# Optimization experiments

Hardware: AMD Instinct MI355X
Metric: run time of the kernel (lower is better)

Reference implementation:

```python
import jax, jax.numpy as jnp
import numpy as np

N_NODES = 100000
N_EDGES = 1600000
F_IN = 64
N_HID = 64
N_CLS = 40
K = 2  # kernel_size, degree-1 open B-spline in 1-D pseudo-coordinate


def setup_inputs() -> dict:
    key = jax.random.key(0)
    ks = jax.random.split(key, 8)
    x = jax.random.normal(ks[0], (N_NODES, F_IN), dtype=jnp.float32)
    edge_index = jax.random.randint(ks[1], (2, N_EDGES), 0, N_NODES, dtype=jnp.int32)
    edge_attr = jax.random.uniform(ks[2], (N_EDGES, 1), dtype=jnp.float32)
    s1 = 1.0 / np.sqrt(F_IN)
    s2 = 1.0 / np.sqrt(N_HID)
    W1 = jax.random.normal(ks[3], (K, F_IN, N_HID), dtype=jnp.float32) * s1
    root1 = jax.random.normal(ks[4], (F_IN, N_HID), dtype=jnp.float32) * s1
    b1 = jnp.zeros((N_HID,), dtype=jnp.float32)
    W2 = jax.random.normal(ks[5], (K, N_HID, N_CLS), dtype=jnp.float32) * s2
    root2 = jax.random.normal(ks[6], (N_HID, N_CLS), dtype=jnp.float32) * s2
    b2 = jnp.zeros((N_CLS,), dtype=jnp.float32)
    return {"x": x, "edge_index": edge_index, "edge_attr": edge_attr,
            "W1": W1, "root1": root1, "b1": b1,
            "W2": W2, "root2": root2, "b2": b2}


def spline_conv(x, src, dst, u, W, root, b):
    """SplineConv, dim=1, kernel_size=2, degree=1, open spline, aggr='mean'.

    Degree-1 open spline with K=2: frac = u*(K-1) = u, basis weights are
    (1-u) at kernel index 0 and u at kernel index 1 for u in [0,1).
    Transform nodes once per kernel index, then gather+mix per edge (cheaper
    and mathematically identical to per-edge matmuls since basis scalars
    commute with the linear map).
    """
    h = jnp.einsum('nf,kfo->kno', x, W)  # [K, N, out]
    b1f = u[:, 0]                        # fractional basis weight, [E]
    msg = (1.0 - b1f)[:, None] * h[0][src] + b1f[:, None] * h[1][src]  # [E, out]
    agg = jax.ops.segment_sum(msg, dst, num_segments=x.shape[0])
    deg = jax.ops.segment_sum(jnp.ones_like(b1f), dst, num_segments=x.shape[0])
    agg = agg / jnp.maximum(deg, 1.0)[:, None]  # mean aggregation
    return agg + x @ root + b


def reference(x, edge_index, edge_attr, W1, root1, b1, W2, root2, b2):
    src, dst = edge_index[0], edge_index[1]
    # eval mode: F.dropout(training=False) is identity
    h = jax.nn.elu(spline_conv(x, src, dst, edge_attr, W1, root1, b1))
    out = spline_conv(h, src, dst, edge_attr, W2, root2, b2)
    return jax.nn.log_softmax(out, axis=1)
```

## Files before the change

### kernel.cpp

```cpp
#include <hip/hip_runtime.h>
#include <math.h>

#define N_NODES 100000
#define N_EDGES 1600000
#define NB_SCAN 391
#define CHUNK 4096
#define NCHA 391
#define NBUK 256
#define DPB 391
#define BSTRIDE 7168
#define TILE_N 25000

typedef __attribute__((ext_vector_type(8))) short bf16x8;
typedef __attribute__((ext_vector_type(4))) float f32x4;

__device__ __forceinline__ unsigned short f2bf(float f) {
    union { float f; unsigned u; } v; v.f = f;
    unsigned r = v.u + 0x7FFF + ((v.u >> 16) & 1);
    return (unsigned short)(r >> 16);
}
__device__ __forceinline__ float bf2f(unsigned short b) {
    union { unsigned u; float f; } v; v.u = ((unsigned)b) << 16;
    return v.f;
}

__global__ void x2bf16_kernel(const float* __restrict__ x,
                              unsigned short* __restrict__ xb) {
    int i = blockIdx.x * 256 + threadIdx.x;
    if (i >= N_NODES * 16) return;
    float4 v = reinterpret_cast<const float4*>(x)[i];
    ushort4 o;
    o.x = f2bf(v.x); o.y = f2bf(v.y); o.z = f2bf(v.z); o.w = f2bf(v.w);
    reinterpret_cast<ushort4*>(xb)[i] = o;
}

__global__ void wt_kernel(const float* __restrict__ W, const float* __restrict__ root,
                          unsigned short* __restrict__ Wt, int COUT, int total) {
    int i = blockIdx.x * 256 + threadIdx.x;
    if (i >= total) return;
    int c = i / 192;
    int k = i - c * 192;
    float v = 0.0f;
    if (c < COUT)
        v = (k < 128) ? W[(k >> 6) * 64 * COUT + (k & 63) * COUT + c]
                      : root[(k - 128) * COUT + c];
    Wt[i] = f2bf(v);
}

__global__ __launch_bounds__(256) void bin_edges(const int* __restrict__ ei,
                                                 const float* __restrict__ ea,
                                                 int* __restrict__ bucket_cur,
                                                 int2* __restrict__ binned) {
    __shared__ int hist[NBUK];
    __shared__ int lbase[NBUK];
    __shared__ int lcur[NBUK];
    __shared__ int gbase[NBUK];
    __shared__ int2 stage[CHUNK];
    __shared__ unsigned char sbkt[CHUNK];
    int tid = threadIdx.x;
    int e0 = blockIdx.x * CHUNK;
    int nval = min(CHUNK, N_EDGES - e0);

    if (tid < NBUK) hist[tid] = 0;
    __syncthreads();
    for (int j = tid; j < nval; j += 256)
        atomicAdd(&hist[ei[N_EDGES + e0 + j] / DPB], 1);
    __syncthreads();
    if (tid < NBUK) lbase[tid] = hist[tid];
    __syncthreads();
    for (int off = 1; off < NBUK; off <<= 1) {
        int v = (tid < NBUK && tid >= off) ? lbase[tid - off] : 0;
        __syncthreads();
        if (tid < NBUK) lbase[tid] += v;
        __syncthreads();
    }
    if (tid < NBUK) {
        int ex = lbase[tid] - hist[tid];
        lbase[tid] = ex;
        lcur[tid]  = ex;
        gbase[tid] = atomicAdd(&bucket_cur[tid], hist[tid]);
    }
    __syncthreads();
    for (int j = tid; j < nval; j += 256) {
        int e = e0 + j;
        int d = ei[N_EDGES + e];
        int b = d / DPB;
        int dl = d - b * DPB;
        float u = ea[e];
        int uq = min((int)(u * 65536.0f + 0.5f), 65535);
        int pos = atomicAdd(&lcur[b], 1);
        stage[pos] = make_int2(ei[e], (uq << 16) | dl);
        sbkt[pos] = (unsigned char)b;
    }
    __syncthreads();
    for (int j = tid; j < nval; j += 256) {
        int b = sbkt[j];
        int gp = gbase[b] + (j - lbase[b]);
        if (gp < BSTRIDE)
            binned[(size_t)b * BSTRIDE + gp] = stage[j];
    }
}

__global__ __launch_bounds__(512) void bucket_sort(const int* __restrict__ bucket_cur,
                                                   const int2* __restrict__ binned,
                                                   int2* __restrict__ rec,
                                                   int* __restrict__ rowptr,
                                                   int* __restrict__ cnt_g) {
    __shared__ int keycnt[1600];
    __shared__ int tsum[512];
    __shared__ int2 stage[BSTRIDE];
    int tid = threadIdx.x;
    int b = blockIdx.x;

    tsum[tid] = (tid < NBUK) ? bucket_cur[tid] : 0;
    __syncthreads();
    for (int off = 1; off < 512; off <<= 1) {
        int v = (tid >= off) ? tsum[tid - off] : 0;
        __syncthreads();
        tsum[tid] += v;
        __syncthreads();
    }
    int base = (b == 0) ? 0 : tsum[b - 1];
    int m = min(bucket_cur[b], BSTRIDE);
    __syncthreads();

    for (int k = tid; k < 1600; k += 512) keycnt[k] = 0;
    __syncthreads();
    const int2* bin = binned + (size_t)b * BSTRIDE;
    for (int j = tid; j < m; j += 512) {
        int2 r = bin[j];
        int key = ((r.y & 1023) << 2) | ((unsigned)r.x / TILE_N);
        atomicAdd(&keycnt[key], 1);
    }
    __syncthreads();
    int k0 = tid << 2;
    int c0 = 0, c1 = 0, c2 = 0, c3 = 0;
    if (tid < DPB) {
        c0 = keycnt[k0]; c1 = keycnt[k0 + 1];
        c2 = keycnt[k0 + 2]; c3 = keycnt[k0 + 3];
    }
    int s4 = c0 + c1 + c2 + c3;
    tsum[tid] = s4;
    __syncthreads();
    for (int off = 1; off < 512; off <<= 1) {
        int v = (tid >= off) ? tsum[tid - off] : 0;
        __syncthreads();
        tsum[tid] += v;
        __syncthreads();
    }
    if (tid < DPB) {
        int p = tsum[tid] - s4;
        int d = b * DPB + tid;
        if (d < N_NODES) {
            rowptr[d] = base + p;
            cnt_g[d]  = s4;
        }
        keycnt[k0] = p;     p += c0;
        keycnt[k0 + 1] = p; p += c1;
        keycnt[k0 + 2] = p; p += c2;
        keycnt[k0 + 3] = p;
    }
    __syncthreads();
    for (int j = tid; j < m; j += 512) {
        int2 r = bin[j];
        int key = ((r.y & 1023) << 2) | ((unsigned)r.x / TILE_N);
        float u = ((unsigned)r.y >> 16) * (1.0f / 65536.0f);
        int pos = atomicAdd(&keycnt[key], 1);
        if (pos < BSTRIDE) stage[pos] = make_int2(r.x, __float_as_int(u));
    }
    __syncthreads();
    for (int j = tid; j < m; j += 512)
        rec[base + j] = stage[j];
}

__global__ __launch_bounds__(256) void pull_agg(
        const int* __restrict__ rowptr, const int* __restrict__ cnt,
        const int2* __restrict__ rec, const unsigned short* __restrict__ featb,
        unsigned short* __restrict__ s01b) {
    int wave_id = (blockIdx.x * 256 + threadIdx.x) >> 6;
    int lane = threadIdx.x & 63;
    int fg = lane & 7;
    int eg = lane >> 3;
    int n = wave_id * 8 + eg;
    bool valid = n < N_NODES;
    int start = 0, deg = 0;
    if (valid) { start = rowptr[n]; deg = cnt[n]; }
    int end = start + deg;
    int il  = end - 1;
    const bf16x8* f8 = reinterpret_cast<const bf16x8*>(featb);
    float s[8], a1[8];
#pragma unroll
    for (int k = 0; k < 8; ++k) { s[k] = 0.0f; a1[k] = 0.0f; }

#define LD(IDX, R, V)                                              \
    { int ic = min(IDX, il); R = rec[ic];                          \
      V = f8[((size_t)(unsigned)R.x << 3) + fg]; }
#define MATH(IDX, R, V)                                            \
    { float mk = (IDX < end) ? 1.0f : 0.0f;                        \
      float um = mk * __int_as_float(R.y);                         \
      _Pragma("unroll")                                            \
      for (int t = 0; t < 8; ++t) {                                \
          float vv = bf2f((unsigned short)V[t]);                   \
          s[t]  = fmaf(mk, vv, s[t]);                              \
          a1[t] = fmaf(um, vv, a1[t]);                             \
      } }

    if (deg > 0) {
        int i = start;
        int2 r0, r1, r2, r3; bf16x8 v0, v1, v2, v3;
        LD(i,     r0, v0)
        LD(i + 1, r1, v1)
        LD(i + 2, r2, v2)
        LD(i + 3, r3, v3)
        while (true) {
            int j = i + 4;
            bool more = j < end;
            int2 q0, q1, q2, q3; bf16x8 w0, w1, w2, w3;
            if (more) {
                LD(j,     q0, w0)
                LD(j + 1, q1, w1)
                LD(j + 2, q2, w2)
                LD(j + 3, q3, w3)
            }
            MATH(i,     r0, v0)
            MATH(i + 1, r1, v1)
            MATH(i + 2, r2, v2)
            MATH(i + 3, r3, v3)
            if (!more) break;
            i = j;
            r0 = q0; v0 = w0; r1 = q1; v1 = w1;
            r2 = q2; v2 = w2; r3 = q3; v3 = w3;
        }
    }
#undef LD
#undef MATH

    if (valid) {
        float dinv = 1.0f / fmaxf((float)deg, 1.0f);
        bf16x8 o0, o1;
#pragma unroll
        for (int k = 0; k < 8; ++k) {
            o0[k] = (short)f2bf((s[k] - a1[k]) * dinv);
            o1[k] = (short)f2bf(a1[k] * dinv);
        }
        *reinterpret_cast<bf16x8*>(s01b + (size_t)n * 128 + fg * 8) = o0;
        *reinterpret_cast<bf16x8*>(s01b + (size_t)n * 128 + 64 + fg * 8) = o1;
    }
}

template<int COUT, int CT, int ACT>
__global__ __launch_bounds__(256) void gemm_mfma(
        const unsigned short* __restrict__ s01b,
        const unsigned short* __restrict__ featb,
        const unsigned short* __restrict__ Wt,
        const float* __restrict__ bias, void* __restrict__ outv) {
    int lane = threadIdx.x & 63;
    int wave = threadIdx.x >> 6;
    int l15  = lane & 15;
    int g    = lane >> 4;
    int nodebase = blockIdx.x * 256 + wave * 64;

    f32x4 acc[4][CT];
#pragma unroll
    for (int rt = 0; rt < 4; ++rt)
#pragma unroll
        for (int ct = 0; ct < CT; ++ct) acc[rt][ct] = (f32x4){0.f, 0.f, 0.f, 0.f};

#pragma unroll
    for (int ks = 0; ks < 6; ++ks) {
        int kk = ks * 32 + g * 8;
        bf16x8 zfrag[4];
#pragma unroll
        for (int rt = 0; rt < 4; ++rt) {
            int n = nodebase + rt * 16 + l15;
            if (n >= N_NODES) n = N_NODES - 1;
            const unsigned short* p = (kk < 128)
                ? (s01b + (size_t)n * 128 + kk)
                : (featb + (size_t)n * 64 + (kk - 128));
            zfrag[rt] = *reinterpret_cast<const bf16x8*>(p);
        }
        bf16x8 wfrag[CT];
#pragma unroll
        for (int ct = 0; ct < CT; ++ct)
            wfrag[ct] = *reinterpret_cast<const bf16x8*>(Wt + (size_t)(ct * 16 + l15) * 192 + kk);
#pragma unroll
        for (int rt = 0; rt < 4; ++rt)
#pragma unroll
            for (int ct = 0; ct < CT; ++ct)
                acc[rt][ct] = __builtin_amdgcn_mfma_f32_16x16x32_bf16(
                    wfrag[ct], zfrag[rt], acc[rt][ct], 0, 0, 0);
    }

    f32x4 bv[CT];
#pragma unroll
    for (int ct = 0; ct < CT; ++ct) {
        int base = ct * 16 + g * 4;
        if (base + 4 <= COUT) {
            float4 b = *reinterpret_cast<const float4*>(bias + base);
            bv[ct] = (f32x4){b.x, b.y, b.z, b.w};
        } else {
            bv[ct] = (f32x4){0.f, 0.f, 0.f, 0.f};
        }
    }

    if (ACT == 1) {
        unsigned short* out = (unsigned short*)outv;
#pragma unroll
        for (int rt = 0; rt < 4; ++rt) {
            int n = nodebase + rt * 16 + l15;
            if (n >= N_NODES) continue;
#pragma unroll
            for (int ct = 0; ct < CT; ++ct) {
                f32x4 v = acc[rt][ct] + bv[ct];
                ushort4 o;
                float e;
                e = v[0]; o.x = f2bf(e > 0.f ? e : expm1f(e));
                e = v[1]; o.y = f2bf(e > 0.f ? e : expm1f(e));
                e = v[2]; o.z = f2bf(e > 0.f ? e : expm1f(e));
                e = v[3]; o.w = f2bf(e > 0.f ? e : expm1f(e));
                *reinterpret_cast<ushort4*>(out + (size_t)n * 64 + ct * 16 + g * 4) = o;
            }
        }
    } else {
        float* out = (float*)outv;
#pragma unroll
        for (int rt = 0; rt < 4; ++rt) {
            int n = nodebase + rt * 16 + l15;
            float v[CT * 4];
            float m = -3.4e38f;
#pragma unroll
            for (int ct = 0; ct < CT; ++ct)
#pragma unroll
                for (int r = 0; r < 4; ++r) {
                    int ch = ct * 16 + g * 4 + r;
                    float t = acc[rt][ct][r] + bv[ct][r];
                    v[ct * 4 + r] = t;
                    if (ch < COUT) m = fmaxf(m, t);
                }
            m = fmaxf(m, __shfl_xor(m, 16));
            m = fmaxf(m, __shfl_xor(m, 32));
            float s = 0.0f;
#pragma unroll
            for (int ct = 0; ct < CT; ++ct)
#pragma unroll
                for (int r = 0; r < 4; ++r) {
                    int ch = ct * 16 + g * 4 + r;
                    if (ch < COUT) s += expf(v[ct * 4 + r] - m);
                }
            s += __shfl_xor(s, 16);
            s += __shfl_xor(s, 32);
            float lse = m + logf(s);
            if (n >= N_NODES) continue;
#pragma unroll
            for (int ct = 0; ct < CT; ++ct) {
                int base = ct * 16 + g * 4;
                if (base + 4 <= COUT) {
                    float4 o;
                    o.x = v[ct * 4 + 0] - lse;
                    o.y = v[ct * 4 + 1] - lse;
                    o.z = v[ct * 4 + 2] - lse;
                    o.w = v[ct * 4 + 3] - lse;
                    *reinterpret_cast<float4*>(out + (size_t)n * COUT + base) = o;
                }
            }
        }
    }
}

extern "C" void kernel_launch(void* const* d_in, const int* in_sizes, int n_in,
                              void* d_out, int out_size, void* d_ws, size_t ws_size,
                              hipStream_t stream) {
    const float* x     = (const float*)d_in[0];
    const int*   ei    = (const int*)d_in[1];
    const float* ea    = (const float*)d_in[2];
    const float* W1    = (const float*)d_in[3];
    const float* root1 = (const float*)d_in[4];
    const float* b1    = (const float*)d_in[5];
    const float* W2    = (const float*)d_in[6];
    const float* root2 = (const float*)d_in[7];
    const float* b2    = (const float*)d_in[8];
    float* out = (float*)d_out;

    char* p = (char*)d_ws;
    int*   bucket_cur = (int*)p;            p += 512 * 4;
    int2*  binned  = (int2*)p;              p += (size_t)NBUK * BSTRIDE * 8;
    int2*  rec     = (int2*)p;              p += (size_t)N_EDGES * 8;
    int*   rowptr  = (int*)p;               p += (size_t)N_NODES * 4;
    int*   cnt     = (int*)p;               p += (size_t)N_NODES * 4;
    unsigned short* s01b = (unsigned short*)p;  p += (size_t)N_NODES * 128 * 2;
    unsigned short* xb   = (unsigned short*)p;  p += (size_t)N_NODES * 64 * 2;
    unsigned short* hprb = (unsigned short*)p;  p += (size_t)N_NODES * 64 * 2;
    unsigned short* Wt1  = (unsigned short*)p;  p += (size_t)64 * 192 * 2;
    unsigned short* Wt2  = (unsigned short*)p;  p += (size_t)48 * 192 * 2;

    x2bf16_kernel<<<(N_NODES * 16) / 256, 256, 0, stream>>>(x, xb);
    wt_kernel<<<48, 256, 0, stream>>>(W1, root1, Wt1, 64, 64 * 192);
    wt_kernel<<<36, 256, 0, stream>>>(W2, root2, Wt2, 40, 48 * 192);
    hipMemsetAsync(bucket_cur, 0, 512 * 4, stream);

    bin_edges<<<NCHA, 256, 0, stream>>>(ei, ea, bucket_cur, binned);
    bucket_sort<<<NBUK, 512, 0, stream>>>(bucket_cur, binned, rec, rowptr, cnt);

    pull_agg<<<(N_NODES + 31) / 32, 256, 0, stream>>>(rowptr, cnt, rec, xb, s01b);
    gemm_mfma<64, 4, 1><<<NB_SCAN, 256, 0, stream>>>(s01b, xb, Wt1, b1, hprb);

    pull_agg<<<(N_NODES + 31) / 32, 256, 0, stream>>>(rowptr, cnt, rec, hprb, s01b);
    gemm_mfma<40, 3, 2><<<NB_SCAN, 256, 0, stream>>>(s01b, hprb, Wt2, b2, out);
}
```

Measured before the change: 163.4 us.

## Degree-bin node permutation for pull_agg and pack edge records to 32 bits

bucket_sort now builds a histogram of node degrees (capped at 63), and two new kernels, scan64 and perm_scatter, produce a permutation that groups nodes of similar degree. pull_agg walks nodes in that order, so the 8 nodes sharing a wave have similar loop trip counts and less divergence. Edge records are also packed into 32 bits (17-bit source plus 15-bit quantised u) instead of an int2, halving record traffic. The cost is two extra small launches, an indirection through perm, coarser quantisation of u, and loss of node locality when reading rowptr and cnt.

New measurement: 168.7 us. +3.3%, slower.

```diff
diff --git a/kernel.cpp b/kernel.cpp
--- a/kernel.cpp
+++ b/kernel.cpp
@@ -103,12 +103,16 @@
 
 __global__ __launch_bounds__(512) void bucket_sort(const int* __restrict__ bucket_cur,
                                                    const int2* __restrict__ binned,
-                                                   int2* __restrict__ rec,
+                                                   unsigned* __restrict__ rec,
                                                    int* __restrict__ rowptr,
-                                                   int* __restrict__ cnt_g) {
+                                                   int* __restrict__ cnt_g,
+                                                   int* __restrict__ bin_cnt,
+                                                   int* __restrict__ bin_rel,
+                                                   int* __restrict__ nodeinfo) {
     __shared__ int keycnt[1600];
     __shared__ int tsum[512];
-    __shared__ int2 stage[BSTRIDE];
+    __shared__ int dh[64];
+    __shared__ unsigned stage[BSTRIDE];
     int tid = threadIdx.x;
     int b = blockIdx.x;
 
@@ -125,6 +129,7 @@
     __syncthreads();
 
     for (int k = tid; k < 1600; k += 512) keycnt[k] = 0;
+    if (tid < 64) dh[tid] = 0;
     __syncthreads();
     const int2* bin = binned + (size_t)b * BSTRIDE;
     for (int j = tid; j < m; j += 512) {
@@ -148,6 +153,8 @@
         tsum[tid] += v;
         __syncthreads();
     }
+    bool isnode = (tid < DPB) && (b * DPB + tid < N_NODES);
+    int binid = 0, lpos = 0;
     if (tid < DPB) {
         int p = tsum[tid] - s4;
         int d = b * DPB + tid;
@@ -159,32 +166,67 @@
         keycnt[k0 + 1] = p; p += c1;
         keycnt[k0 + 2] = p; p += c2;
         keycnt[k0 + 3] = p;
-    }
-    __syncthreads();
+        if (isnode) {
+            binid = min(s4, 63);
+            lpos = atomicAdd(&dh[binid], 1);
+        }
+    }
+    __syncthreads();
+    if (tid < 64) bin_rel[b * 64 + tid] = atomicAdd(&bin_cnt[tid], dh[tid]);
+    if (isnode) nodeinfo[b * DPB + tid] = (binid << 9) | lpos;
     for (int j = tid; j < m; j += 512) {
         int2 r = bin[j];
         int key = ((r.y & 1023) << 2) | ((unsigned)r.x / TILE_N);
-        float u = ((unsigned)r.y >> 16) * (1.0f / 65536.0f);
+        unsigned uq15 = ((unsigned)r.y >> 17);
         int pos = atomicAdd(&keycnt[key], 1);
-        if (pos < BSTRIDE) stage[pos] = make_int2(r.x, __float_as_int(u));
+        if (pos < BSTRIDE) stage[pos] = ((unsigned)r.x << 15) | uq15;
     }
     __syncthreads();
     for (int j = tid; j < m; j += 512)
         rec[base + j] = stage[j];
 }
 
+__global__ void scan64(const int* __restrict__ bin_cnt, int* __restrict__ bin_base) {
+    __shared__ int s[64];
+    int t = threadIdx.x;
+    int v = bin_cnt[t];
+    s[t] = v;
+    __syncthreads();
+    for (int off = 1; off < 64; off <<= 1) {
+        int w = (t >= off) ? s[t - off] : 0;
+        __syncthreads();
+        s[t] += w;
+        __syncthreads();
+    }
+    bin_base[t] = s[t] - v;
+}
+
+__global__ void perm_scatter(const int* __restrict__ nodeinfo,
+                             const int* __restrict__ bin_rel,
+                             const int* __restrict__ bin_base,
+                             int* __restrict__ perm) {
+    int n = blockIdx.x * 256 + threadIdx.x;
+    if (n >= N_NODES) return;
+    int b = n / DPB;
+    int info = nodeinfo[n];
+    int bin = info >> 9;
+    int lpos = info & 511;
+    perm[bin_base[bin] + bin_rel[b * 64 + bin] + lpos] = n;
+}
+
 __global__ __launch_bounds__(256) void pull_agg(
         const int* __restrict__ rowptr, const int* __restrict__ cnt,
-        const int2* __restrict__ rec, const unsigned short* __restrict__ featb,
+        const int* __restrict__ perm, const unsigned* __restrict__ rec,
+        const unsigned short* __restrict__ featb,
         unsigned short* __restrict__ s01b) {
-    int wave_id = (blockIdx.x * 256 + threadIdx.x) >> 6;
+    int gid = (blockIdx.x * 256 + threadIdx.x) >> 6;
     int lane = threadIdx.x & 63;
     int fg = lane & 7;
     int eg = lane >> 3;
-    int n = wave_id * 8 + eg;
-    bool valid = n < N_NODES;
-    int start = 0, deg = 0;
-    if (valid) { start = rowptr[n]; deg = cnt[n]; }
+    int idx = gid * 8 + eg;
+    bool valid = idx < N_NODES;
+    int n = 0, start = 0, deg = 0;
+    if (valid) { n = perm[idx]; start = rowptr[n]; deg = cnt[n]; }
     int end = start + deg;
     int il  = end - 1;
     const bf16x8* f8 = reinterpret_cast<const bf16x8*>(featb);
@@ -194,10 +236,10 @@
 
 #define LD(IDX, R, V)                                              \
     { int ic = min(IDX, il); R = rec[ic];                          \
-      V = f8[((size_t)(unsigned)R.x << 3) + fg]; }
+      V = f8[((size_t)(R >> 15) << 3) + fg]; }
 #define MATH(IDX, R, V)                                            \
     { float mk = (IDX < end) ? 1.0f : 0.0f;                        \
-      float um = mk * __int_as_float(R.y);                         \
+      float um = mk * (float)(R & 0x7FFFu) * (1.0f / 32768.0f);    \
       _Pragma("unroll")                                            \
       for (int t = 0; t < 8; ++t) {                                \
           float vv = bf2f((unsigned short)V[t]);                   \
@@ -207,7 +249,7 @@
 
     if (deg > 0) {
         int i = start;
-        int2 r0, r1, r2, r3; bf16x8 v0, v1, v2, v3;
+        unsigned r0, r1, r2, r3; bf16x8 v0, v1, v2, v3;
         LD(i,     r0, v0)
         LD(i + 1, r1, v1)
         LD(i + 2, r2, v2)
@@ -215,7 +257,7 @@
         while (true) {
             int j = i + 4;
             bool more = j < end;
-            int2 q0, q1, q2, q3; bf16x8 w0, w1, w2, w3;
+            unsigned q0, q1, q2, q3; bf16x8 w0, w1, w2, w3;
             if (more) {
                 LD(j,     q0, w0)
                 LD(j + 1, q1, w1)
@@ -383,8 +425,13 @@
 
     char* p = (char*)d_ws;
     int*   bucket_cur = (int*)p;            p += 512 * 4;
+    int*   bin_cnt  = (int*)p;              p += 64 * 4;
+    int*   bin_base = (int*)p;              p += 64 * 4;
+    int*   bin_rel  = (int*)p;              p += (size_t)NBUK * 64 * 4;
+    int*   nodeinfo = (int*)p;              p += (size_t)N_NODES * 4;
+    int*   perm     = (int*)p;              p += (size_t)N_NODES * 4;
     int2*  binned  = (int2*)p;              p += (size_t)NBUK * BSTRIDE * 8;
-    int2*  rec     = (int2*)p;              p += (size_t)N_EDGES * 8;
+    unsigned* rec  = (unsigned*)p;          p += (size_t)N_EDGES * 4;
     int*   rowptr  = (int*)p;               p += (size_t)N_NODES * 4;
     int*   cnt     = (int*)p;               p += (size_t)N_NODES * 4;
     unsigned short* s01b = (unsigned short*)p;  p += (size_t)N_NODES * 128 * 2;
@@ -396,14 +443,17 @@
     x2bf16_kernel<<<(N_NODES * 16) / 256, 256, 0, stream>>>(x, xb);
     wt_kernel<<<48, 256, 0, stream>>>(W1, root1, Wt1, 64, 64 * 192);
     wt_kernel<<<36, 256, 0, stream>>>(W2, root2, Wt2, 40, 48 * 192);
-    hipMemsetAsync(bucket_cur, 0, 512 * 4, stream);
+    hipMemsetAsync(bucket_cur, 0, (512 + 64) * 4, stream);
 
     bin_edges<<<NCHA, 256, 0, stream>>>(ei, ea, bucket_cur, binned);
-    bucket_sort<<<NBUK, 512, 0, stream>>>(bucket_cur, binned, rec, rowptr, cnt);
-
-    pull_agg<<<(N_NODES + 31) / 32, 256, 0, stream>>>(rowptr, cnt, rec, xb, s01b);
+    bucket_sort<<<NBUK, 512, 0, stream>>>(bucket_cur, binned, rec, rowptr, cnt,
+                                          bin_cnt, bin_rel, nodeinfo);
+    scan64<<<1, 64, 0, stream>>>(bin_cnt, bin_base);
+    perm_scatter<<<NB_SCAN, 256, 0, stream>>>(nodeinfo, bin_rel, bin_base, perm);
+
+    pull_agg<<<(N_NODES + 31) / 32, 256, 0, stream>>>(rowptr, cnt, perm, rec, xb, s01b);
     gemm_mfma<64, 4, 1><<<NB_SCAN, 256, 0, stream>>>(s01b, xb, Wt1, b1, hprb);
 
-    pull_agg<<<(N_NODES + 31) / 32, 256, 0, stream>>>(rowptr, cnt, rec, hprb, s01b);
+    pull_agg<<<(N_NODES + 31) / 32, 256, 0, stream>>>(rowptr, cnt, perm, rec, hprb, s01b);
     gemm_mfma<40, 3, 2><<<NB_SCAN, 256, 0, stream>>>(s01b, hprb, Wt2, b2, out);
 }
```
